# Optimization experiments

Measured on AMD Instinct MI355X. Metric: run time of the kernel, lower is better.

Reference implementation:

```python
import jax, jax.numpy as jnp
import numpy as np

N = 50000       # num nodes
E = 600000      # num edges
IN = 128        # in_channels
H = 4           # heads
C = 32          # out_channels per head
B = 3           # num bends (Bezier control points)
NEG_SLOPE = 0.2


def setup_inputs() -> dict:
    key = jax.random.key(0)
    ks = jax.random.split(key, 6)
    x = jax.random.normal(ks[0], (N, IN), dtype=jnp.float32)
    edge_index = jax.random.randint(ks[1], (2, E), 0, N)
    # Bezier coefficients at t=0.5 for a 3-point curve: [0.25, 0.5, 0.25]
    coeffs_t = jnp.array([0.25, 0.5, 0.25], dtype=jnp.float32)
    glorot_w = float(np.sqrt(2.0) * np.sqrt(6.0 / (H * C + IN)))
    glorot_a = float(np.sqrt(2.0) * np.sqrt(6.0 / (1 + C)))
    lin_weight = jax.random.uniform(ks[2], (B, H * C, IN), jnp.float32, -glorot_w, glorot_w)
    lin_bias = jnp.zeros((B, H * C), dtype=jnp.float32)
    att_src = jax.random.uniform(ks[3], (B, 1, H, C), jnp.float32, -glorot_a, glorot_a)
    att_dst = jax.random.uniform(ks[4], (B, 1, H, C), jnp.float32, -glorot_a, glorot_a)
    return {"x": x, "edge_index": edge_index, "coeffs_t": coeffs_t,
            "lin_weight": lin_weight, "lin_bias": lin_bias,
            "att_src": att_src, "att_dst": att_dst}


def reference(x, edge_index, coeffs_t, lin_weight, lin_bias, att_src, att_dst):
    # Bezier parameter interpolation: weighted sum over bends
    W = jnp.einsum('b,boi->oi', coeffs_t, lin_weight)      # [H*C, IN]
    bias = jnp.einsum('b,bo->o', coeffs_t, lin_bias)       # [H*C]
    a_src = jnp.einsum('b,bqhc->qhc', coeffs_t, att_src)   # [1,H,C]
    a_dst = jnp.einsum('b,bqhc->qhc', coeffs_t, att_dst)   # [1,H,C]

    n = x.shape[0]
    xt = (x @ W.T + bias).reshape(n, H, C)                 # [N,H,C]
    alpha_src = jnp.sum(xt * a_src, axis=-1)               # [N,H]
    alpha_dst = jnp.sum(xt * a_dst, axis=-1)               # [N,H]

    row, col = edge_index[0], edge_index[1]
    alpha = alpha_src[row] + alpha_dst[col]                # [E,H]
    alpha = jax.nn.leaky_relu(alpha, NEG_SLOPE)

    # scatter-softmax over incoming edges of each target node (col)
    amax = jax.ops.segment_max(alpha, col, num_segments=n)  # [N,H]
    ex = jnp.exp(alpha - amax[col])                         # [E,H]
    denom = jax.ops.segment_sum(ex, col, num_segments=n)    # [N,H]
    alpha = ex / (denom[col] + 1e-16)                       # [E,H]

    # weighted neighbor aggregation (edge-parallel segment reduction)
    msg = xt[row] * alpha[..., None]                        # [E,H,C]
    out = jax.ops.segment_sum(msg, col, num_segments=n)     # [N,H,C]
    return out.reshape(n, H * C)                            # concat=True
```

## Files before the change

kernel.cpp:

```cpp
#include <hip/hip_runtime.h>
#include <hip/hip_bf16.h>

#define GAT_IN   128
#define GAT_OUT  128
#define GAT_H    4
#define GAT_C    32
#define NEG_SLOPE 0.2f
#define BUCKET   96

typedef __attribute__((ext_vector_type(8))) short bf16x8;
typedef __attribute__((ext_vector_type(4))) float f32x4;
union U4 { uint4 u; bf16x8 v; };

static __device__ __forceinline__ unsigned int pack_bf16(float lo, float hi) {
    __hip_bfloat16 a = __float2bfloat16(lo);
    __hip_bfloat16 b = __float2bfloat16(hi);
    unsigned short ua = *reinterpret_cast<unsigned short*>(&a);
    unsigned short ub = *reinterpret_cast<unsigned short*>(&b);
    return (unsigned int)ua | ((unsigned int)ub << 16);
}

__global__ __launch_bounds__(256) void interp_kernel(
    const float* __restrict__ coeffs,
    const float* __restrict__ lw,
    const float* __restrict__ lb,
    const float* __restrict__ asr,
    const float* __restrict__ ads,
    unsigned int* __restrict__ wfrag,
    float* __restrict__ biasc,
    float* __restrict__ asrc, float* __restrict__ adst,
    int* __restrict__ cnt, int n)
{
    int i = blockIdx.x * 256 + threadIdx.x;
    float c0 = coeffs[0], c1 = coeffs[1], c2 = coeffs[2];
    if (i < 8192) {
        int lane = (i >> 2) & 63;
        int nk   = i >> 8;
        int jw   = i & 3;
        int nt = nk >> 2, ks = nk & 3;
        int o = nt * 16 + (lane & 15);
        int k = ks * 32 + (lane >> 4) * 8 + jw * 2;
        int idx = o * 128 + k;
        float w0 = c0 * lw[idx]     + c1 * lw[16384 + idx]     + c2 * lw[32768 + idx];
        float w1 = c0 * lw[idx + 1] + c1 * lw[16384 + idx + 1] + c2 * lw[32768 + idx + 1];
        wfrag[i] = pack_bf16(w0, w1);
    }
    if (i < 128) {
        biasc[i] = c0 * lb[i]  + c1 * lb[128 + i]  + c2 * lb[256 + i];
        asrc[i]  = c0 * asr[i] + c1 * asr[128 + i] + c2 * asr[256 + i];
        adst[i]  = c0 * ads[i] + c1 * ads[128 + i] + c2 * ads[256 + i];
    }
    if (i < n) cnt[i] = 0;
}

__global__ __launch_bounds__(256) void gemm_alpha_kernel(
    const float* __restrict__ x,
    const unsigned int* __restrict__ wfrag,
    const float* __restrict__ biasc,
    const float* __restrict__ asrc,
    const float* __restrict__ adst,
    unsigned int* __restrict__ xtb,
    float* __restrict__ alpha_src,
    float* __restrict__ alpha_dst,
    int n)
{
    __shared__ __align__(16) float C[64 * 132];
    int tid  = threadIdx.x;
    int lane = tid & 63;
    int wave = tid >> 6;
    int quad = lane >> 4;
    int lm   = lane & 15;
    int m0   = blockIdx.x * 64 + wave * 16;

    f32x4 acc[8];
    #pragma unroll
    for (int t = 0; t < 8; ++t) acc[t] = (f32x4){0.f, 0.f, 0.f, 0.f};

    int arow = m0 + lm; if (arow >= n) arow = n - 1;
    const float4* xr = (const float4*)(x + (size_t)arow * 128 + quad * 8);
    const uint4*  wf = (const uint4*)wfrag;

    #pragma unroll
    for (int ks = 0; ks < 4; ++ks) {
        float4 a0 = xr[ks * 8 + 0];
        float4 a1 = xr[ks * 8 + 1];
        U4 af;
        af.u.x = pack_bf16(a0.x, a0.y);
        af.u.y = pack_bf16(a0.z, a0.w);
        af.u.z = pack_bf16(a1.x, a1.y);
        af.u.w = pack_bf16(a1.z, a1.w);
        #pragma unroll
        for (int nt = 0; nt < 8; ++nt) {
            U4 bf; bf.u = wf[(nt * 4 + ks) * 64 + lane];
            acc[nt] = __builtin_amdgcn_mfma_f32_16x16x32_bf16(
                af.v, bf.v, acc[nt], 0, 0, 0);
        }
    }

    #pragma unroll
    for (int nt = 0; nt < 8; ++nt) {
        int col = nt * 16 + lm;
        #pragma unroll
        for (int r = 0; r < 4; ++r) {
            int rowl = wave * 16 + quad * 4 + r;
            C[rowl * 132 + col] = acc[nt][r];
        }
    }
    __syncthreads();

    int rowl = wave * 16 + (lane >> 2);
    int seg  = lane & 3;
    int mrow = blockIdx.x * 64 + rowl;
    if (mrow < n) {
        const float4* cb = (const float4*)(C + rowl * 132 + seg * 32);
        const float4* bb = (const float4*)(biasc + seg * 32);
        const float4* sb = (const float4*)(asrc + seg * 32);
        const float4* db = (const float4*)(adst + seg * 32);
        float s = 0.f, d = 0.f;
        unsigned int ow[16];
        #pragma unroll
        for (int q = 0; q < 8; ++q) {
            float4 v = cb[q];
            float4 b = bb[q];
            v.x += b.x; v.y += b.y; v.z += b.z; v.w += b.w;
            float4 as = sb[q], ad = db[q];
            s += v.x * as.x + v.y * as.y + v.z * as.z + v.w * as.w;
            d += v.x * ad.x + v.y * ad.y + v.z * ad.z + v.w * ad.w;
            ow[q * 2 + 0] = pack_bf16(v.x, v.y);
            ow[q * 2 + 1] = pack_bf16(v.z, v.w);
        }
        alpha_src[mrow * 4 + seg] = s;
        alpha_dst[mrow * 4 + seg] = d;
        uint4* xo = (uint4*)(xtb + (size_t)mrow * 64 + seg * 16);
        #pragma unroll
        for (int q4 = 0; q4 < 4; ++q4)
            xo[q4] = make_uint4(ow[q4 * 4], ow[q4 * 4 + 1],
                                ow[q4 * 4 + 2], ow[q4 * 4 + 3]);
    }
}

__global__ __launch_bounds__(256) void bucket_kernel(
    const int* __restrict__ ei, int* __restrict__ cnt,
    int* __restrict__ esrc, int ne)
{
    int e = blockIdx.x * 256 + threadIdx.x;
    if (e >= ne) return;
    int row = ei[e], col = ei[ne + e];
    int pos = atomicAdd(&cnt[col], 1);
    if (pos < BUCKET) esrc[col * BUCKET + pos] = row;
}

__device__ __forceinline__ void edge_math2(
    unsigned int r, unsigned int h, unsigned int sl, float ad,
    const unsigned int* __restrict__ xtb,
    const float* __restrict__ alpha_src,
    float& den, float4& acc)
{
    float as = alpha_src[(r << 2) | h];
    uint2 u = *(const uint2*)(xtb + (r << 6) + (sl << 1));
    float a = as + ad;
    a = fmaxf(a, NEG_SLOPE * a);
    float ex = __expf(a);
    den += ex;
    acc.x = fmaf(ex, __uint_as_float(u.x << 16), acc.x);
    acc.y = fmaf(ex, __uint_as_float(u.x & 0xFFFF0000u), acc.y);
    acc.z = fmaf(ex, __uint_as_float(u.y << 16), acc.z);
    acc.w = fmaf(ex, __uint_as_float(u.y & 0xFFFF0000u), acc.w);
}

__global__ __launch_bounds__(256) void agg_kernel(
    const int* __restrict__ cnt,
    const int* __restrict__ esrc,
    const unsigned int* __restrict__ xtb,
    const float* __restrict__ alpha_src,
    const float* __restrict__ alpha_dst,
    float* __restrict__ out,
    int n)
{
    int wave = threadIdx.x >> 6;
    unsigned int lane = threadIdx.x & 63;
    unsigned int sub = lane >> 5;
    unsigned int sl  = lane & 31;
    int node = blockIdx.x * 8 + wave * 2 + (int)sub;
    bool active = node < n;
    int nodec = active ? node : 0;
    unsigned int h = sl >> 3;

    float ad = alpha_dst[((unsigned)nodec << 2) | h];
    const int* eb = esrc + nodec * BUCKET;
    int m = active ? cnt[nodec] : 0; if (m > BUCKET) m = BUCKET;

    float4 acc = make_float4(0.f, 0.f, 0.f, 0.f);
    float den = 0.f;
    int j = 0;
    for (; j + 8 <= m; j += 8) {
        int4 ra = *(const int4*)(eb + j);
        int4 rb = *(const int4*)(eb + j + 4);
        float as0 = alpha_src[((unsigned)ra.x << 2) | h];
        float as1 = alpha_src[((unsigned)ra.y << 2) | h];
        float as2 = alpha_src[((unsigned)ra.z << 2) | h];
        float as3 = alpha_src[((unsigned)ra.w << 2) | h];
        float as4 = alpha_src[((unsigned)rb.x << 2) | h];
        float as5 = alpha_src[((unsigned)rb.y << 2) | h];
        float as6 = alpha_src[((unsigned)rb.z << 2) | h];
        float as7 = alpha_src[((unsigned)rb.w << 2) | h];
        uint2 u0 = *(const uint2*)(xtb + (((unsigned)ra.x << 6) + (sl << 1)));
        uint2 u1 = *(const uint2*)(xtb + (((unsigned)ra.y << 6) + (sl << 1)));
        uint2 u2 = *(const uint2*)(xtb + (((unsigned)ra.z << 6) + (sl << 1)));
        uint2 u3 = *(const uint2*)(xtb + (((unsigned)ra.w << 6) + (sl << 1)));
        uint2 u4 = *(const uint2*)(xtb + (((unsigned)rb.x << 6) + (sl << 1)));
        uint2 u5 = *(const uint2*)(xtb + (((unsigned)rb.y << 6) + (sl << 1)));
        uint2 u6 = *(const uint2*)(xtb + (((unsigned)rb.z << 6) + (sl << 1)));
        uint2 u7 = *(const uint2*)(xtb + (((unsigned)rb.w << 6) + (sl << 1)));
        float a0 = fmaxf(as0 + ad, NEG_SLOPE * (as0 + ad));
        float a1 = fmaxf(as1 + ad, NEG_SLOPE * (as1 + ad));
        float a2 = fmaxf(as2 + ad, NEG_SLOPE * (as2 + ad));
        float a3 = fmaxf(as3 + ad, NEG_SLOPE * (as3 + ad));
        float a4 = fmaxf(as4 + ad, NEG_SLOPE * (as4 + ad));
        float a5 = fmaxf(as5 + ad, NEG_SLOPE * (as5 + ad));
        float a6 = fmaxf(as6 + ad, NEG_SLOPE * (as6 + ad));
        float a7 = fmaxf(as7 + ad, NEG_SLOPE * (as7 + ad));
        float e0 = __expf(a0), e1 = __expf(a1), e2 = __expf(a2), e3 = __expf(a3);
        float e4 = __expf(a4), e5 = __expf(a5), e6 = __expf(a6), e7 = __expf(a7);
        den += ((e0 + e1) + (e2 + e3)) + ((e4 + e5) + (e6 + e7));
        acc.x = fmaf(e0, __uint_as_float(u0.x << 16),
                fmaf(e1, __uint_as_float(u1.x << 16),
                fmaf(e2, __uint_as_float(u2.x << 16),
                fmaf(e3, __uint_as_float(u3.x << 16),
                fmaf(e4, __uint_as_float(u4.x << 16),
                fmaf(e5, __uint_as_float(u5.x << 16),
                fmaf(e6, __uint_as_float(u6.x << 16),
                fmaf(e7, __uint_as_float(u7.x << 16), acc.x))))))));
        acc.y = fmaf(e0, __uint_as_float(u0.x & 0xFFFF0000u),
                fmaf(e1, __uint_as_float(u1.x & 0xFFFF0000u),
                fmaf(e2, __uint_as_float(u2.x & 0xFFFF0000u),
                fmaf(e3, __uint_as_float(u3.x & 0xFFFF0000u),
                fmaf(e4, __uint_as_float(u4.x & 0xFFFF0000u),
                fmaf(e5, __uint_as_float(u5.x & 0xFFFF0000u),
                fmaf(e6, __uint_as_float(u6.x & 0xFFFF0000u),
                fmaf(e7, __uint_as_float(u7.x & 0xFFFF0000u), acc.y))))))));
        acc.z = fmaf(e0, __uint_as_float(u0.y << 16),
                fmaf(e1, __uint_as_float(u1.y << 16),
                fmaf(e2, __uint_as_float(u2.y << 16),
                fmaf(e3, __uint_as_float(u3.y << 16),
                fmaf(e4, __uint_as_float(u4.y << 16),
                fmaf(e5, __uint_as_float(u5.y << 16),
                fmaf(e6, __uint_as_float(u6.y << 16),
                fmaf(e7, __uint_as_float(u7.y << 16), acc.z))))))));
        acc.w = fmaf(e0, __uint_as_float(u0.y & 0xFFFF0000u),
                fmaf(e1, __uint_as_float(u1.y & 0xFFFF0000u),
                fmaf(e2, __uint_as_float(u2.y & 0xFFFF0000u),
                fmaf(e3, __uint_as_float(u3.y & 0xFFFF0000u),
                fmaf(e4, __uint_as_float(u4.y & 0xFFFF0000u),
                fmaf(e5, __uint_as_float(u5.y & 0xFFFF0000u),
                fmaf(e6, __uint_as_float(u6.y & 0xFFFF0000u),
                fmaf(e7, __uint_as_float(u7.y & 0xFFFF0000u), acc.w))))))));
    }
    if (j + 4 <= m) {
        int4 ra = *(const int4*)(eb + j);
        edge_math2(ra.x, h, sl, ad, xtb, alpha_src, den, acc);
        edge_math2(ra.y, h, sl, ad, xtb, alpha_src, den, acc);
        edge_math2(ra.z, h, sl, ad, xtb, alpha_src, den, acc);
        edge_math2(ra.w, h, sl, ad, xtb, alpha_src, den, acc);
        j += 4;
    }
    for (; j < m; ++j)
        edge_math2(eb[j], h, sl, ad, xtb, alpha_src, den, acc);

    if (active) {
        float inv = 1.0f / (den + 1e-16f);
        ((float4*)out)[((unsigned)node << 5) | sl] =
            make_float4(acc.x * inv, acc.y * inv, acc.z * inv, acc.w * inv);
    }
}

extern "C" void kernel_launch(void* const* d_in, const int* in_sizes, int n_in,
                              void* d_out, int out_size, void* d_ws, size_t ws_size,
                              hipStream_t stream)
{
    const float* x      = (const float*)d_in[0];
    const int*   ei     = (const int*)  d_in[1];
    const float* coeffs = (const float*)d_in[2];
    const float* lw     = (const float*)d_in[3];
    const float* lb     = (const float*)d_in[4];
    const float* asr    = (const float*)d_in[5];
    const float* ads    = (const float*)d_in[6];
    float* out = (float*)d_out;

    int n  = in_sizes[0] / GAT_IN;
    int ne = in_sizes[1] / 2;

    float* ws        = (float*)d_ws;
    unsigned int* wfrag = (unsigned int*)ws;
    float* biasc     = ws + 16384;
    float* asrc      = ws + 16512;
    float* adst      = ws + 16640;
    unsigned int* xtb = (unsigned int*)(ws + 16768);
    float* alpha_src = (float*)(xtb + (size_t)n * 64);
    float* alpha_dst = alpha_src + (size_t)n * 4;
    int*   cnt       = (int*)(alpha_dst + (size_t)n * 4);
    int*   esrc      = cnt + n;

    int zb = (n + 255) / 256; if (zb < 64) zb = 64;
    interp_kernel<<<zb, 256, 0, stream>>>(coeffs, lw, lb, asr, ads,
                                          wfrag, biasc, asrc, adst, cnt, n);
    gemm_alpha_kernel<<<(n + 63) / 64, 256, 0, stream>>>(
        x, wfrag, biasc, asrc, adst, xtb, alpha_src, alpha_dst, n);
    bucket_kernel<<<(ne + 255) / 256, 256, 0, stream>>>(ei, cnt, esrc, ne);
    agg_kernel<<<(n + 7) / 8, 256, 0, stream>>>(
        cnt, esrc, xtb, alpha_src, alpha_dst, out, n);
}
```

Baseline: 168.7 us.

## Fuse bucketing into interp kernel and use masked 16-wide aggregation loop

```diff
diff --git a/kernel.cpp b/kernel.cpp
--- a/kernel.cpp
+++ b/kernel.cpp
@@ -20,7 +20,9 @@
     return (unsigned int)ua | ((unsigned int)ub << 16);
 }
 
-__global__ __launch_bounds__(256) void interp_kernel(
+__global__ __launch_bounds__(256) void bucket_interp_kernel(
+    const int* __restrict__ ei, int* __restrict__ cnt,
+    int* __restrict__ esrc, int ne,
     const float* __restrict__ coeffs,
     const float* __restrict__ lw,
     const float* __restrict__ lb,
@@ -28,12 +30,12 @@
     const float* __restrict__ ads,
     unsigned int* __restrict__ wfrag,
     float* __restrict__ biasc,
-    float* __restrict__ asrc, float* __restrict__ adst,
-    int* __restrict__ cnt, int n)
-{
-    int i = blockIdx.x * 256 + threadIdx.x;
-    float c0 = coeffs[0], c1 = coeffs[1], c2 = coeffs[2];
-    if (i < 8192) {
+    float* __restrict__ asrc, float* __restrict__ adst)
+{
+    int b = blockIdx.x;
+    if (b < 32) {
+        int i = b * 256 + threadIdx.x;
+        float c0 = coeffs[0], c1 = coeffs[1], c2 = coeffs[2];
         int lane = (i >> 2) & 63;
         int nk   = i >> 8;
         int jw   = i & 3;
@@ -44,13 +46,19 @@
         float w0 = c0 * lw[idx]     + c1 * lw[16384 + idx]     + c2 * lw[32768 + idx];
         float w1 = c0 * lw[idx + 1] + c1 * lw[16384 + idx + 1] + c2 * lw[32768 + idx + 1];
         wfrag[i] = pack_bf16(w0, w1);
-    }
-    if (i < 128) {
-        biasc[i] = c0 * lb[i]  + c1 * lb[128 + i]  + c2 * lb[256 + i];
-        asrc[i]  = c0 * asr[i] + c1 * asr[128 + i] + c2 * asr[256 + i];
-        adst[i]  = c0 * ads[i] + c1 * ads[128 + i] + c2 * ads[256 + i];
-    }
-    if (i < n) cnt[i] = 0;
+        if (b == 0 && threadIdx.x < 128) {
+            int t = threadIdx.x;
+            biasc[t] = c0 * lb[t]  + c1 * lb[128 + t]  + c2 * lb[256 + t];
+            asrc[t]  = c0 * asr[t] + c1 * asr[128 + t] + c2 * asr[256 + t];
+            adst[t]  = c0 * ads[t] + c1 * ads[128 + t] + c2 * ads[256 + t];
+        }
+        return;
+    }
+    int e = (b - 32) * 256 + threadIdx.x;
+    if (e >= ne) return;
+    int row = ei[e], col = ei[ne + e];
+    int pos = atomicAdd(&cnt[col], 1);
+    if (pos < BUCKET) esrc[col * BUCKET + pos] = row;
 }
 
 __global__ __launch_bounds__(256) void gemm_alpha_kernel(
@@ -139,35 +147,6 @@
     }
 }
 
-__global__ __launch_bounds__(256) void bucket_kernel(
-    const int* __restrict__ ei, int* __restrict__ cnt,
-    int* __restrict__ esrc, int ne)
-{
-    int e = blockIdx.x * 256 + threadIdx.x;
-    if (e >= ne) return;
-    int row = ei[e], col = ei[ne + e];
-    int pos = atomicAdd(&cnt[col], 1);
-    if (pos < BUCKET) esrc[col * BUCKET + pos] = row;
-}
-
-__device__ __forceinline__ void edge_math2(
-    unsigned int r, unsigned int h, unsigned int sl, float ad,
-    const unsigned int* __restrict__ xtb,
-    const float* __restrict__ alpha_src,
-    float& den, float4& acc)
-{
-    float as = alpha_src[(r << 2) | h];
-    uint2 u = *(const uint2*)(xtb + (r << 6) + (sl << 1));
-    float a = as + ad;
-    a = fmaxf(a, NEG_SLOPE * a);
-    float ex = __expf(a);
-    den += ex;
-    acc.x = fmaf(ex, __uint_as_float(u.x << 16), acc.x);
-    acc.y = fmaf(ex, __uint_as_float(u.x & 0xFFFF0000u), acc.y);
-    acc.z = fmaf(ex, __uint_as_float(u.y << 16), acc.z);
-    acc.w = fmaf(ex, __uint_as_float(u.y & 0xFFFF0000u), acc.w);
-}
-
 __global__ __launch_bounds__(256) void agg_kernel(
     const int* __restrict__ cnt,
     const int* __restrict__ esrc,
@@ -192,80 +171,47 @@
 
     float4 acc = make_float4(0.f, 0.f, 0.f, 0.f);
     float den = 0.f;
-    int j = 0;
-    for (; j + 8 <= m; j += 8) {
+
+    for (int j = 0; j < m; j += 16) {
+        int rem = m - j;
         int4 ra = *(const int4*)(eb + j);
         int4 rb = *(const int4*)(eb + j + 4);
-        float as0 = alpha_src[((unsigned)ra.x << 2) | h];
-        float as1 = alpha_src[((unsigned)ra.y << 2) | h];
-        float as2 = alpha_src[((unsigned)ra.z << 2) | h];
-        float as3 = alpha_src[((unsigned)ra.w << 2) | h];
-        float as4 = alpha_src[((unsigned)rb.x << 2) | h];
-        float as5 = alpha_src[((unsigned)rb.y << 2) | h];
-        float as6 = alpha_src[((unsigned)rb.z << 2) | h];
-        float as7 = alpha_src[((unsigned)rb.w << 2) | h];
-        uint2 u0 = *(const uint2*)(xtb + (((unsigned)ra.x << 6) + (sl << 1)));
-        uint2 u1 = *(const uint2*)(xtb + (((unsigned)ra.y << 6) + (sl << 1)));
-        uint2 u2 = *(const uint2*)(xtb + (((unsigned)ra.z << 6) + (sl << 1)));
-        uint2 u3 = *(const uint2*)(xtb + (((unsigned)ra.w << 6) + (sl << 1)));
-        uint2 u4 = *(const uint2*)(xtb + (((unsigned)rb.x << 6) + (sl << 1)));
-        uint2 u5 = *(const uint2*)(xtb + (((unsigned)rb.y << 6) + (sl << 1)));
-        uint2 u6 = *(const uint2*)(xtb + (((unsigned)rb.z << 6) + (sl << 1)));
-        uint2 u7 = *(const uint2*)(xtb + (((unsigned)rb.w << 6) + (sl << 1)));
-        float a0 = fmaxf(as0 + ad, NEG_SLOPE * (as0 + ad));
-        float a1 = fmaxf(as1 + ad, NEG_SLOPE * (as1 + ad));
-        float a2 = fmaxf(as2 + ad, NEG_SLOPE * (as2 + ad));
-        float a3 = fmaxf(as3 + ad, NEG_SLOPE * (as3 + ad));
-        float a4 = fmaxf(as4 + ad, NEG_SLOPE * (as4 + ad));
-        float a5 = fmaxf(as5 + ad, NEG_SLOPE * (as5 + ad));
-        float a6 = fmaxf(as6 + ad, NEG_SLOPE * (as6 + ad));
-        float a7 = fmaxf(as7 + ad, NEG_SLOPE * (as7 + ad));
-        float e0 = __expf(a0), e1 = __expf(a1), e2 = __expf(a2), e3 = __expf(a3);
-        float e4 = __expf(a4), e5 = __expf(a5), e6 = __expf(a6), e7 = __expf(a7);
-        den += ((e0 + e1) + (e2 + e3)) + ((e4 + e5) + (e6 + e7));
-        acc.x = fmaf(e0, __uint_as_float(u0.x << 16),
-                fmaf(e1, __uint_as_float(u1.x << 16),
-                fmaf(e2, __uint_as_float(u2.x << 16),
-                fmaf(e3, __uint_as_float(u3.x << 16),
-                fmaf(e4, __uint_as_float(u4.x << 16),
-                fmaf(e5, __uint_as_float(u5.x << 16),
-                fmaf(e6, __uint_as_float(u6.x << 16),
-                fmaf(e7, __uint_as_float(u7.x << 16), acc.x))))))));
-        acc.y = fmaf(e0, __uint_as_float(u0.x & 0xFFFF0000u),
-                fmaf(e1, __uint_as_float(u1.x & 0xFFFF0000u),
-                fmaf(e2, __uint_as_float(u2.x & 0xFFFF0000u),
-                fmaf(e3, __uint_as_float(u3.x & 0xFFFF0000u),
-                fmaf(e4, __uint_as_float(u4.x & 0xFFFF0000u),
-                fmaf(e5, __uint_as_float(u5.x & 0xFFFF0000u),
-                fmaf(e6, __uint_as_float(u6.x & 0xFFFF0000u),
-                fmaf(e7, __uint_as_float(u7.x & 0xFFFF0000u), acc.y))))))));
-        acc.z = fmaf(e0, __uint_as_float(u0.y << 16),
-                fmaf(e1, __uint_as_float(u1.y << 16),
-                fmaf(e2, __uint_as_float(u2.y << 16),
-                fmaf(e3, __uint_as_float(u3.y << 16),
-                fmaf(e4, __uint_as_float(u4.y << 16),
-                fmaf(e5, __uint_as_float(u5.y << 16),
-                fmaf(e6, __uint_as_float(u6.y << 16),
-                fmaf(e7, __uint_as_float(u7.y << 16), acc.z))))))));
-        acc.w = fmaf(e0, __uint_as_float(u0.y & 0xFFFF0000u),
-                fmaf(e1, __uint_as_float(u1.y & 0xFFFF0000u),
-                fmaf(e2, __uint_as_float(u2.y & 0xFFFF0000u),
-                fmaf(e3, __uint_as_float(u3.y & 0xFFFF0000u),
-                fmaf(e4, __uint_as_float(u4.y & 0xFFFF0000u),
-                fmaf(e5, __uint_as_float(u5.y & 0xFFFF0000u),
-                fmaf(e6, __uint_as_float(u6.y & 0xFFFF0000u),
-                fmaf(e7, __uint_as_float(u7.y & 0xFFFF0000u), acc.w))))))));
-    }
-    if (j + 4 <= m) {
-        int4 ra = *(const int4*)(eb + j);
-        edge_math2(ra.x, h, sl, ad, xtb, alpha_src, den, acc);
-        edge_math2(ra.y, h, sl, ad, xtb, alpha_src, den, acc);
-        edge_math2(ra.z, h, sl, ad, xtb, alpha_src, den, acc);
-        edge_math2(ra.w, h, sl, ad, xtb, alpha_src, den, acc);
-        j += 4;
-    }
-    for (; j < m; ++j)
-        edge_math2(eb[j], h, sl, ad, xtb, alpha_src, den, acc);
+        int4 rc = *(const int4*)(eb + j + 8);
+        int4 rd = *(const int4*)(eb + j + 12);
+        int r[16];
+        r[0]=ra.x;  r[1]=ra.y;  r[2]=ra.z;  r[3]=ra.w;
+        r[4]=rb.x;  r[5]=rb.y;  r[6]=rb.z;  r[7]=rb.w;
+        r[8]=rc.x;  r[9]=rc.y;  r[10]=rc.z; r[11]=rc.w;
+        r[12]=rd.x; r[13]=rd.y; r[14]=rd.z; r[15]=rd.w;
+        #pragma unroll
+        for (int t = 0; t < 16; ++t) r[t] = (t < rem) ? r[t] : 0;
+
+        float as[16];
+        #pragma unroll
+        for (int t = 0; t < 16; ++t)
+            as[t] = alpha_src[(((unsigned)r[t]) << 2) | h];
+        uint2 u[16];
+        #pragma unroll
+        for (int t = 0; t < 16; ++t)
+            u[t] = *(const uint2*)(xtb + ((((unsigned)r[t]) << 6) + (sl << 1)));
+
+        float e[16];
+        #pragma unroll
+        for (int t = 0; t < 16; ++t) {
+            float a = as[t] + ad;
+            a = fmaxf(a, NEG_SLOPE * a);
+            float ex = __expf(a);
+            e[t] = (t < rem) ? ex : 0.f;
+            den += e[t];
+        }
+        #pragma unroll
+        for (int t = 0; t < 16; ++t) {
+            acc.x = fmaf(e[t], __uint_as_float(u[t].x << 16),          acc.x);
+            acc.y = fmaf(e[t], __uint_as_float(u[t].x & 0xFFFF0000u),  acc.y);
+            acc.z = fmaf(e[t], __uint_as_float(u[t].y << 16),          acc.z);
+            acc.w = fmaf(e[t], __uint_as_float(u[t].y & 0xFFFF0000u),  acc.w);
+        }
+    }
 
     if (active) {
         float inv = 1.0f / (den + 1e-16f);
@@ -301,12 +247,11 @@
     int*   cnt       = (int*)(alpha_dst + (size_t)n * 4);
     int*   esrc      = cnt + n;
 
-    int zb = (n + 255) / 256; if (zb < 64) zb = 64;
-    interp_kernel<<<zb, 256, 0, stream>>>(coeffs, lw, lb, asr, ads,
-                                          wfrag, biasc, asrc, adst, cnt, n);
+    hipMemsetAsync(cnt, 0, (size_t)n * sizeof(int), stream);
+    bucket_interp_kernel<<<32 + (ne + 255) / 256, 256, 0, stream>>>(
+        ei, cnt, esrc, ne, coeffs, lw, lb, asr, ads, wfrag, biasc, asrc, adst);
     gemm_alpha_kernel<<<(n + 63) / 64, 256, 0, stream>>>(
         x, wfrag, biasc, asrc, adst, xtb, alpha_src, alpha_dst, n);
-    bucket_kernel<<<(ne + 255) / 256, 256, 0, stream>>>(ei, cnt, esrc, ne);
     agg_kernel<<<(n + 7) / 8, 256, 0, stream>>>(
         cnt, esrc, xtb, alpha_src, alpha_dst, out, n);
 }
```

New measurement: 167.6 us. Within noise of the previous version (-0.7%).
